# Performance work log

Hardware: AMD Instinct MI355X
Metric: run time of the kernel (lower is better)

## Reference

```python
import jax, jax.numpy as jnp
import numpy as np

N_POINTS = 2_000_000
NUM_GRAPHS = 16384
HID = 40  # ffn_param hidden_layer_size
SLOPE = 0.01  # torch default LeakyReLU negative slope


def _w(key, fan_in, fan_out):
    return jax.random.normal(key, (fan_in, fan_out), dtype=jnp.float32) / np.sqrt(fan_in)


def ffn(x, W1, W2, final_linear=False):
    # FFN with n_layers=2, bias=False, hidden=40; dropout is identity in eval.
    h = jax.nn.leaky_relu(x @ W1, SLOPE)
    h = h @ W2
    return h if final_linear else jax.nn.leaky_relu(h, SLOPE)


def setup_inputs() -> dict:
    key = jax.random.key(0)
    ks = jax.random.split(key, 10)
    x = jax.random.normal(ks[0], (N_POINTS, 3), dtype=jnp.float32)
    batch = jnp.sort(jax.random.randint(ks[1], (N_POINTS,), 0, NUM_GRAPHS)).astype(jnp.int64)
    return {
        "x": x,
        "batch": batch,
        # EPiC emb_nn: FFN(3 -> 5)
        "W_emb1": _w(ks[2], 3, HID), "W_emb2": _w(ks[3], HID, 5),
        # EPiC global_nn: FFN(5 -> 4)
        "W_glob1": _w(ks[4], 5, HID), "W_glob2": _w(ks[5], HID, 4),
        # EPiC out_nn: FFN(5+4 -> 32)
        "W_out1": _w(ks[6], 9, HID), "W_out2": _w(ks[7], HID, 32),
        # disc: FFN(32 -> 1, final_linear=True)
        "W_disc1": _w(ks[8], 32, HID), "W_disc2": _w(ks[9], HID, 1),
    }


def reference(x, batch, W_emb1, W_emb2, W_glob1, W_glob2, W_out1, W_out2, W_disc1, W_disc2):
    # EPiC block
    xe = ffn(x, W_emb1, W_emb2)                                   # [N, 5]
    x_aggr = jax.ops.segment_sum(xe, batch, num_segments=NUM_GRAPHS,
                                 indices_are_sorted=True)          # [B, 5]
    x_global = ffn(x_aggr, W_glob1, W_glob2)                       # [B, 4]
    xo = ffn(jnp.concatenate([xe, x_global[batch]], axis=-1),
             W_out1, W_out2)                                       # [N, 32]
    # global pool + final discriminator head
    pooled = jax.ops.segment_sum(xo, batch, num_segments=NUM_GRAPHS,
                                 indices_are_sorted=True)          # [B, 32]
    return ffn(pooled, W_disc1, W_disc2, final_linear=True)        # [B, 1]
```

## Files before the change

kernel.cpp:

```cpp
#include <hip/hip_runtime.h>
#include <hip/hip_bf16.h>

#define N_POINTS   2000000
#define NUM_GRAPHS 16384
#define HID        40
#define SLOPE      0.01f
#define TILE       256
#define NTILES     ((N_POINTS + TILE - 1) / TILE)
#define AROW       20
#define XOS        260

typedef __attribute__((ext_vector_type(8))) short short8;
typedef __attribute__((ext_vector_type(4))) float fx4;

__device__ __forceinline__ float lrelu(float v) { return v > 0.f ? v : SLOPE * v; }

__global__ __launch_bounds__(256) void k_emb_aggr(
    const float* __restrict__ x, const int* __restrict__ batch,
    const float* __restrict__ We1, const float* __restrict__ We2,
    float* __restrict__ x_aggr)
{
    __shared__ float sWe1[3 * HID];
    __shared__ float sWe2T[5 * HID];
    __shared__ __align__(16) float xeT[5 * XOS];
    __shared__ __align__(16) int   sb[TILE];

    int tid = threadIdx.x;
    for (int k = tid; k < 3 * HID; k += 256) sWe1[k] = We1[k];
    for (int k = tid; k < 5 * HID; k += 256) sWe2T[k] = We2[(k % HID) * 5 + k / HID];
    __syncthreads();

    for (int t = blockIdx.x; t < NTILES; t += gridDim.x) {
        int i = t * TILE + tid;
        bool v = i < N_POINTS;
        int ic = v ? i : (N_POINTS - 1);
        float x0 = x[ic * 3 + 0], x1 = x[ic * 3 + 1], x2 = x[ic * 3 + 2];
        int b = v ? batch[ic] : -1;
        sb[tid] = b;

        float h[HID];
        const float4* W1r = (const float4*)sWe1;
#pragma unroll
        for (int j4 = 0; j4 < HID / 4; ++j4) {
            float4 wa = W1r[j4], wb = W1r[10 + j4], wc = W1r[20 + j4];
            float wav[4] = {wa.x, wa.y, wa.z, wa.w};
            float wbv[4] = {wb.x, wb.y, wb.z, wb.w};
            float wcv[4] = {wc.x, wc.y, wc.z, wc.w};
#pragma unroll
            for (int k = 0; k < 4; ++k)
                h[j4 * 4 + k] = lrelu(x0 * wav[k] + x1 * wbv[k] + x2 * wcv[k]);
        }
#pragma unroll
        for (int c = 0; c < 5; ++c) {
            const float4* wr = (const float4*)&sWe2T[c * HID];
            float s = 0.f;
#pragma unroll
            for (int j4 = 0; j4 < HID / 4; ++j4) {
                float4 w = wr[j4];
                s += h[j4 * 4 + 0] * w.x + h[j4 * 4 + 1] * w.y + h[j4 * 4 + 2] * w.z + h[j4 * 4 + 3] * w.w;
            }
            xeT[c * XOS + tid] = lrelu(s);
        }
        __syncthreads();

        if (tid < 40) {
            int ch = tid >> 3, chunk = tid & 7;
            float acc = 0.f;
            int cur = sb[chunk * 32];
#pragma unroll
            for (int g = 0; g < 8; ++g) {
                float4 v4 = *(const float4*)&xeT[ch * XOS + chunk * 32 + g * 4];
                int4   n4 = *(const int4*)&sb[chunk * 32 + g * 4];
                float vv[4] = {v4.x, v4.y, v4.z, v4.w};
                int   nn[4] = {n4.x, n4.y, n4.z, n4.w};
#pragma unroll
                for (int k = 0; k < 4; ++k) {
                    if (nn[k] != cur) {
                        if (cur >= 0) atomicAdd(&x_aggr[cur * 5 + ch], acc);
                        cur = nn[k];
                        acc = vv[k];
                    } else {
                        acc += vv[k];
                    }
                }
            }
            if (cur >= 0) atomicAdd(&x_aggr[cur * 5 + ch], acc);
        }
        __syncthreads();
    }
}

__global__ __launch_bounds__(256) void k_global(
    const float* __restrict__ x_aggr,
    const float* __restrict__ Wg1, const float* __restrict__ Wg2,
    const float* __restrict__ Wo1,
    float* __restrict__ g_contrib)
{
    __shared__ float sWg1[5 * HID];
    __shared__ float sWg2[HID * 4];
    __shared__ float sWo1g[4 * HID];
    for (int k = threadIdx.x; k < 5 * HID; k += 256) sWg1[k] = Wg1[k];
    for (int k = threadIdx.x; k < HID * 4; k += 256) sWg2[k] = Wg2[k];
    for (int k = threadIdx.x; k < 4 * HID; k += 256) sWo1g[k] = Wo1[5 * HID + k];
    __syncthreads();

    int bg = blockIdx.x * 256 + threadIdx.x;
    if (bg >= NUM_GRAPHS) return;

    float a[5];
#pragma unroll
    for (int c = 0; c < 5; ++c) a[c] = x_aggr[bg * 5 + c];

    float h[HID];
#pragma unroll
    for (int j = 0; j < HID; ++j) {
        float s = 0.f;
#pragma unroll
        for (int c = 0; c < 5; ++c) s += a[c] * sWg1[c * HID + j];
        h[j] = lrelu(s);
    }
    float g[4];
#pragma unroll
    for (int c = 0; c < 4; ++c) {
        float s = 0.f;
#pragma unroll
        for (int j = 0; j < HID; ++j) s += h[j] * sWg2[j * 4 + c];
        g[c] = lrelu(s);
    }
#pragma unroll
    for (int j = 0; j < HID; ++j) {
        float s = 0.f;
#pragma unroll
        for (int c = 0; c < 4; ++c) s += g[c] * sWo1g[c * HID + j];
        g_contrib[bg * HID + j] = s;
    }
}

__global__ __launch_bounds__(256, 4) void k_out_pool(
    const float* __restrict__ x, const int* __restrict__ batch,
    const float* __restrict__ We1, const float* __restrict__ We2,
    const float* __restrict__ Wo1, const float* __restrict__ Wo2,
    const float* __restrict__ g_contrib,
    float* __restrict__ pooled)
{
    __shared__ __align__(16) unsigned int uLds[32 * XOS];
    __shared__ __align__(16) int sb[TILE];
    __shared__ float sWe1[3 * HID];
    __shared__ float sWe2T[5 * HID];
    __shared__ float sWo1[5 * HID];

    int tid = threadIdx.x;
    for (int k = tid; k < 3 * HID; k += 256) sWe1[k] = We1[k];
    for (int k = tid; k < 5 * HID; k += 256) sWe2T[k] = We2[(k % HID) * 5 + k / HID];
    for (int k = tid; k < 5 * HID; k += 256) sWo1[k] = Wo1[k];

    int lane = tid & 63;
    int l16 = lane & 15, quad = lane >> 4;

    short8 bfrag[2][2];
#pragma unroll
    for (int nt = 0; nt < 2; ++nt) {
#pragma unroll
        for (int ks = 0; ks < 2; ++ks) {
#pragma unroll
            for (int j = 0; j < 8; ++j) {
                int kk = ks * 32 + quad * 8 + j;
                float w = (kk < HID) ? Wo2[kk * 32 + nt * 16 + l16] : 0.f;
                __hip_bfloat16 hb = __float2bfloat16(w);
                bfrag[nt][ks][j] = *(short*)&hb;
            }
        }
    }
    short8 zfrag = {0, 0, 0, 0, 0, 0, 0, 0};
    __syncthreads();

    for (int t = blockIdx.x; t < NTILES; t += gridDim.x) {
        int i = t * TILE + tid;
        bool v = i < N_POINTS;
        int ic = v ? i : (N_POINTS - 1);
        float x0 = x[ic * 3 + 0], x1 = x[ic * 3 + 1], x2 = x[ic * 3 + 2];
        int b = v ? batch[ic] : -1;
        sb[tid] = b;

        float h[HID];
        const float4* W1r = (const float4*)sWe1;
#pragma unroll
        for (int j4 = 0; j4 < HID / 4; ++j4) {
            float4 wa = W1r[j4], wb = W1r[10 + j4], wc = W1r[20 + j4];
            float wav[4] = {wa.x, wa.y, wa.z, wa.w};
            float wbv[4] = {wb.x, wb.y, wb.z, wb.w};
            float wcv[4] = {wc.x, wc.y, wc.z, wc.w};
#pragma unroll
            for (int k = 0; k < 4; ++k)
                h[j4 * 4 + k] = lrelu(x0 * wav[k] + x1 * wbv[k] + x2 * wcv[k]);
        }
        float xe[5];
#pragma unroll
        for (int c = 0; c < 5; ++c) {
            const float4* wr = (const float4*)&sWe2T[c * HID];
            float s = 0.f;
#pragma unroll
            for (int j4 = 0; j4 < HID / 4; ++j4) {
                float4 w = wr[j4];
                s += h[j4 * 4 + 0] * w.x + h[j4 * 4 + 1] * w.y + h[j4 * 4 + 2] * w.z + h[j4 * 4 + 3] * w.w;
            }
            xe[c] = lrelu(s);
        }

        const float4* gc4 = (const float4*)(g_contrib + (size_t)(v ? b : 0) * HID);
        float h1v[HID];
#pragma unroll
        for (int j4 = 0; j4 < HID / 4; ++j4) {
            float4 g = gc4[j4];
            float sv[4] = {g.x, g.y, g.z, g.w};
#pragma unroll
            for (int c = 0; c < 5; ++c) {
                float4 w = ((const float4*)&sWo1[c * HID])[j4];
                float wv[4] = {w.x, w.y, w.z, w.w};
#pragma unroll
                for (int k = 0; k < 4; ++k) sv[k] += xe[c] * wv[k];
            }
#pragma unroll
            for (int k = 0; k < 4; ++k) h1v[j4 * 4 + k] = lrelu(sv[k]);
        }

        unsigned int* row = &uLds[tid * AROW];
#pragma unroll
        for (int c = 0; c < 5; ++c) {
            __hip_bfloat162 p0 = __float22bfloat162_rn(make_float2(h1v[8 * c + 0], h1v[8 * c + 1]));
            __hip_bfloat162 p1 = __float22bfloat162_rn(make_float2(h1v[8 * c + 2], h1v[8 * c + 3]));
            __hip_bfloat162 p2 = __float22bfloat162_rn(make_float2(h1v[8 * c + 4], h1v[8 * c + 5]));
            __hip_bfloat162 p3 = __float22bfloat162_rn(make_float2(h1v[8 * c + 6], h1v[8 * c + 7]));
            uint4 u;
            u.x = *(unsigned int*)&p0; u.y = *(unsigned int*)&p1;
            u.z = *(unsigned int*)&p2; u.w = *(unsigned int*)&p3;
            *(uint4*)(row + c * 4) = u;
        }

        fx4 xov[4][2];
#pragma unroll
        for (int m = 0; m < 4; ++m) {
            int mt = (tid >> 6) * 4 + m;
            const unsigned int* arow = &uLds[(mt * 16 + l16) * AROW];
            short8 a0 = *(const short8*)(arow + quad * 4);
            short8 a1 = (quad == 0) ? *(const short8*)(arow + 16) : zfrag;
#pragma unroll
            for (int nt = 0; nt < 2; ++nt) {
                fx4 acc = {0.f, 0.f, 0.f, 0.f};
                acc = __builtin_amdgcn_mfma_f32_16x16x32_bf16(a0, bfrag[nt][0], acc, 0, 0, 0);
                acc = __builtin_amdgcn_mfma_f32_16x16x32_bf16(a1, bfrag[nt][1], acc, 0, 0, 0);
#pragma unroll
                for (int r = 0; r < 4; ++r) acc[r] = lrelu(acc[r]);
                xov[m][nt] = acc;
            }
        }
        __syncthreads();

        float* xoT = (float*)uLds;
#pragma unroll
        for (int m = 0; m < 4; ++m) {
            int mt = (tid >> 6) * 4 + m;
#pragma unroll
            for (int nt = 0; nt < 2; ++nt) {
                int ch = nt * 16 + l16;
                int pt = mt * 16 + quad * 4;
                *(fx4*)&xoT[ch * XOS + pt] = xov[m][nt];
            }
        }
        __syncthreads();

        {
            int ch = tid & 31, chunk = tid >> 5;
            float acc = 0.f;
            int cur = sb[chunk * 32];
#pragma unroll
            for (int g = 0; g < 8; ++g) {
                float4 v4 = *(const float4*)&xoT[ch * XOS + chunk * 32 + g * 4];
                int4   n4 = *(const int4*)&sb[chunk * 32 + g * 4];
                float vv[4] = {v4.x, v4.y, v4.z, v4.w};
                int   nn[4] = {n4.x, n4.y, n4.z, n4.w};
#pragma unroll
                for (int k = 0; k < 4; ++k) {
                    if (nn[k] != cur) {
                        if (cur >= 0) atomicAdd(&pooled[cur * 32 + ch], acc);
                        cur = nn[k];
                        acc = vv[k];
                    } else {
                        acc += vv[k];
                    }
                }
            }
            if (cur >= 0) atomicAdd(&pooled[cur * 32 + ch], acc);
        }
        __syncthreads();
    }
}

__global__ __launch_bounds__(256) void k_disc(
    const float* __restrict__ pooled,
    const float* __restrict__ Wd1, const float* __restrict__ Wd2,
    float* __restrict__ out)
{
    __shared__ float sWd1T[HID * 32];
    __shared__ float sWd2[HID];
    for (int k = threadIdx.x; k < 32 * HID; k += 256) sWd1T[k] = Wd1[(k % 32) * HID + k / 32];
    for (int k = threadIdx.x; k < HID; k += 256) sWd2[k] = Wd2[k];
    __syncthreads();

    int bg = blockIdx.x * 256 + threadIdx.x;
    if (bg >= NUM_GRAPHS) return;

    float p[32];
    const float4* pp = (const float4*)(pooled + (size_t)bg * 32);
#pragma unroll
    for (int c4 = 0; c4 < 8; ++c4) {
        float4 vv = pp[c4];
        p[c4 * 4 + 0] = vv.x; p[c4 * 4 + 1] = vv.y; p[c4 * 4 + 2] = vv.z; p[c4 * 4 + 3] = vv.w;
    }

    float acc = 0.f;
#pragma unroll
    for (int j = 0; j < HID; ++j) {
        const float4* wr = (const float4*)&sWd1T[j * 32];
        float s = 0.f;
#pragma unroll
        for (int c4 = 0; c4 < 8; ++c4) {
            float4 w = wr[c4];
            s += p[c4 * 4 + 0] * w.x + p[c4 * 4 + 1] * w.y + p[c4 * 4 + 2] * w.z + p[c4 * 4 + 3] * w.w;
        }
        acc += lrelu(s) * sWd2[j];
    }
    out[bg] = acc;
}

extern "C" void kernel_launch(void* const* d_in, const int* in_sizes, int n_in,
                              void* d_out, int out_size, void* d_ws, size_t ws_size,
                              hipStream_t stream) {
    const float* x     = (const float*)d_in[0];
    const int*   batch = (const int*)  d_in[1];
    const float* We1   = (const float*)d_in[2];
    const float* We2   = (const float*)d_in[3];
    const float* Wg1   = (const float*)d_in[4];
    const float* Wg2   = (const float*)d_in[5];
    const float* Wo1   = (const float*)d_in[6];
    const float* Wo2   = (const float*)d_in[7];
    const float* Wd1   = (const float*)d_in[8];
    const float* Wd2   = (const float*)d_in[9];
    float* out = (float*)d_out;

    float* x_aggr    = (float*)d_ws;
    float* pooled    = x_aggr + NUM_GRAPHS * 5;
    float* g_contrib = pooled + NUM_GRAPHS * 32;

    hipMemsetAsync(d_ws, 0, (size_t)NUM_GRAPHS * (5 + 32) * sizeof(float), stream);

    int gblk = (NUM_GRAPHS + 255) / 256;
    k_emb_aggr<<<2048, 256, 0, stream>>>(x, batch, We1, We2, x_aggr);
    k_global <<<gblk, 256, 0, stream>>>(x_aggr, Wg1, Wg2, Wo1, g_contrib);
    k_out_pool<<<1024, 256, 0, stream>>>(x, batch, We1, We2, Wo1, Wo2, g_contrib, pooled);
    k_disc   <<<gblk, 256, 0, stream>>>(pooled, Wd1, Wd2, out);
}
```

Baseline: 218.7 us.

## Cache bf16 embedding outputs between kernels and process two points per thread

```diff
diff --git a/kernel.cpp b/kernel.cpp
--- a/kernel.cpp
+++ b/kernel.cpp
@@ -5,6 +5,11 @@
 #define NUM_GRAPHS 16384
 #define HID        40
 #define SLOPE      0.01f
+
+#define TILE_A     512
+#define NT_A       ((N_POINTS + TILE_A - 1) / TILE_A)
+#define XESA       584
+
 #define TILE       256
 #define NTILES     ((N_POINTS + TILE - 1) / TILE)
 #define AROW       20
@@ -14,79 +19,105 @@
 typedef __attribute__((ext_vector_type(4))) float fx4;
 
 __device__ __forceinline__ float lrelu(float v) { return v > 0.f ? v : SLOPE * v; }
-
-__global__ __launch_bounds__(256) void k_emb_aggr(
+__device__ __forceinline__ int padidx(int p) { return p + ((p >> 5) << 2); }
+__device__ __forceinline__ unsigned short f2bf(float f) {
+    __hip_bfloat16 h = __float2bfloat16(f);
+    return *(unsigned short*)&h;
+}
+__device__ __forceinline__ float bf2f(unsigned short u) {
+    unsigned int v = ((unsigned int)u) << 16;
+    return __uint_as_float(v);
+}
+
+__global__ __launch_bounds__(256, 2) void k_emb_aggr(
     const float* __restrict__ x, const int* __restrict__ batch,
     const float* __restrict__ We1, const float* __restrict__ We2,
-    float* __restrict__ x_aggr)
+    float* __restrict__ x_aggr, unsigned short* __restrict__ xe_out, int use_xe)
 {
-    __shared__ float sWe1[3 * HID];
-    __shared__ float sWe2T[5 * HID];
-    __shared__ __align__(16) float xeT[5 * XOS];
-    __shared__ __align__(16) int   sb[TILE];
+    __shared__ __align__(16) float sWe1[3 * HID];
+    __shared__ __align__(16) float sWe2T[5 * HID];
+    __shared__ __align__(16) float xeT[5 * XESA];
+    __shared__ __align__(16) int   sbp[XESA];
 
     int tid = threadIdx.x;
     for (int k = tid; k < 3 * HID; k += 256) sWe1[k] = We1[k];
     for (int k = tid; k < 5 * HID; k += 256) sWe2T[k] = We2[(k % HID) * 5 + k / HID];
     __syncthreads();
 
-    for (int t = blockIdx.x; t < NTILES; t += gridDim.x) {
-        int i = t * TILE + tid;
-        bool v = i < N_POINTS;
-        int ic = v ? i : (N_POINTS - 1);
-        float x0 = x[ic * 3 + 0], x1 = x[ic * 3 + 1], x2 = x[ic * 3 + 2];
-        int b = v ? batch[ic] : -1;
-        sb[tid] = b;
-
-        float h[HID];
-        const float4* W1r = (const float4*)sWe1;
+    int base = blockIdx.x * TILE_A;
+    int p0 = base + tid, p1 = base + 256 + tid;
+    bool v0 = p0 < N_POINTS, v1 = p1 < N_POINTS;
+    int i0 = v0 ? p0 : (N_POINTS - 1), i1 = v1 ? p1 : (N_POINTS - 1);
+    float a0 = x[i0 * 3 + 0], a1 = x[i0 * 3 + 1], a2 = x[i0 * 3 + 2];
+    float c0 = x[i1 * 3 + 0], c1 = x[i1 * 3 + 1], c2 = x[i1 * 3 + 2];
+    int b0 = v0 ? batch[i0] : -1;
+    int b1 = v1 ? batch[i1] : -1;
+    sbp[padidx(tid)] = b0;
+    sbp[padidx(256 + tid)] = b1;
+
+    float h0[HID], h1[HID];
+    const float4* W1r = (const float4*)sWe1;
+#pragma unroll
+    for (int j4 = 0; j4 < HID / 4; ++j4) {
+        float4 wa = W1r[j4], wb = W1r[10 + j4], wc = W1r[20 + j4];
+        float wav[4] = {wa.x, wa.y, wa.z, wa.w};
+        float wbv[4] = {wb.x, wb.y, wb.z, wb.w};
+        float wcv[4] = {wc.x, wc.y, wc.z, wc.w};
+#pragma unroll
+        for (int k = 0; k < 4; ++k) {
+            int j = j4 * 4 + k;
+            h0[j] = lrelu(a0 * wav[k] + a1 * wbv[k] + a2 * wcv[k]);
+            h1[j] = lrelu(c0 * wav[k] + c1 * wbv[k] + c2 * wcv[k]);
+        }
+    }
+
+#pragma unroll
+    for (int c = 0; c < 5; ++c) {
+        const float4* wr = (const float4*)&sWe2T[c * HID];
+        float s0 = 0.f, s1 = 0.f;
 #pragma unroll
         for (int j4 = 0; j4 < HID / 4; ++j4) {
-            float4 wa = W1r[j4], wb = W1r[10 + j4], wc = W1r[20 + j4];
-            float wav[4] = {wa.x, wa.y, wa.z, wa.w};
-            float wbv[4] = {wb.x, wb.y, wb.z, wb.w};
-            float wcv[4] = {wc.x, wc.y, wc.z, wc.w};
-#pragma unroll
-            for (int k = 0; k < 4; ++k)
-                h[j4 * 4 + k] = lrelu(x0 * wav[k] + x1 * wbv[k] + x2 * wcv[k]);
-        }
-#pragma unroll
-        for (int c = 0; c < 5; ++c) {
-            const float4* wr = (const float4*)&sWe2T[c * HID];
-            float s = 0.f;
-#pragma unroll
-            for (int j4 = 0; j4 < HID / 4; ++j4) {
-                float4 w = wr[j4];
-                s += h[j4 * 4 + 0] * w.x + h[j4 * 4 + 1] * w.y + h[j4 * 4 + 2] * w.z + h[j4 * 4 + 3] * w.w;
-            }
-            xeT[c * XOS + tid] = lrelu(s);
-        }
-        __syncthreads();
-
-        if (tid < 40) {
-            int ch = tid >> 3, chunk = tid & 7;
-            float acc = 0.f;
-            int cur = sb[chunk * 32];
-#pragma unroll
-            for (int g = 0; g < 8; ++g) {
-                float4 v4 = *(const float4*)&xeT[ch * XOS + chunk * 32 + g * 4];
-                int4   n4 = *(const int4*)&sb[chunk * 32 + g * 4];
-                float vv[4] = {v4.x, v4.y, v4.z, v4.w};
-                int   nn[4] = {n4.x, n4.y, n4.z, n4.w};
-#pragma unroll
-                for (int k = 0; k < 4; ++k) {
-                    if (nn[k] != cur) {
-                        if (cur >= 0) atomicAdd(&x_aggr[cur * 5 + ch], acc);
-                        cur = nn[k];
-                        acc = vv[k];
-                    } else {
-                        acc += vv[k];
-                    }
+            float4 w = wr[j4];
+            float wv[4] = {w.x, w.y, w.z, w.w};
+#pragma unroll
+            for (int k = 0; k < 4; ++k) {
+                s0 += h0[j4 * 4 + k] * wv[k];
+                s1 += h1[j4 * 4 + k] * wv[k];
+            }
+        }
+        float e0 = v0 ? lrelu(s0) : 0.f;
+        float e1 = v1 ? lrelu(s1) : 0.f;
+        xeT[c * XESA + padidx(tid)] = e0;
+        xeT[c * XESA + padidx(256 + tid)] = e1;
+        if (use_xe) {
+            if (v0) xe_out[(size_t)c * N_POINTS + p0] = f2bf(e0);
+            if (v1) xe_out[(size_t)c * N_POINTS + p1] = f2bf(e1);
+        }
+    }
+    __syncthreads();
+
+    if (tid < 80) {
+        int ch = tid >> 4, chunk = tid & 15;
+        float acc = 0.f;
+        int cur = sbp[chunk * 36];
+#pragma unroll
+        for (int g = 0; g < 8; ++g) {
+            float4 v4 = *(const float4*)&xeT[ch * XESA + chunk * 36 + g * 4];
+            int4   n4 = *(const int4*)&sbp[chunk * 36 + g * 4];
+            float vv[4] = {v4.x, v4.y, v4.z, v4.w};
+            int   nn[4] = {n4.x, n4.y, n4.z, n4.w};
+#pragma unroll
+            for (int k = 0; k < 4; ++k) {
+                if (nn[k] != cur) {
+                    if (cur >= 0) atomicAdd(&x_aggr[cur * 5 + ch], acc);
+                    cur = nn[k];
+                    acc = vv[k];
+                } else {
+                    acc += vv[k];
                 }
             }
-            if (cur >= 0) atomicAdd(&x_aggr[cur * 5 + ch], acc);
-        }
-        __syncthreads();
+        }
+        if (cur >= 0) atomicAdd(&x_aggr[cur * 5 + ch], acc);
     }
 }
 
@@ -141,6 +172,7 @@
     const float* __restrict__ We1, const float* __restrict__ We2,
     const float* __restrict__ Wo1, const float* __restrict__ Wo2,
     const float* __restrict__ g_contrib,
+    const unsigned short* __restrict__ xe_in, int use_xe,
     float* __restrict__ pooled)
 {
     __shared__ __align__(16) unsigned int uLds[32 * XOS];
@@ -166,8 +198,7 @@
             for (int j = 0; j < 8; ++j) {
                 int kk = ks * 32 + quad * 8 + j;
                 float w = (kk < HID) ? Wo2[kk * 32 + nt * 16 + l16] : 0.f;
-                __hip_bfloat16 hb = __float2bfloat16(w);
-                bfrag[nt][ks][j] = *(short*)&hb;
+                bfrag[nt][ks][j] = (short)f2bf(w);
             }
         }
     }
@@ -178,37 +209,42 @@
         int i = t * TILE + tid;
         bool v = i < N_POINTS;
         int ic = v ? i : (N_POINTS - 1);
-        float x0 = x[ic * 3 + 0], x1 = x[ic * 3 + 1], x2 = x[ic * 3 + 2];
         int b = v ? batch[ic] : -1;
         sb[tid] = b;
 
-        float h[HID];
-        const float4* W1r = (const float4*)sWe1;
-#pragma unroll
-        for (int j4 = 0; j4 < HID / 4; ++j4) {
-            float4 wa = W1r[j4], wb = W1r[10 + j4], wc = W1r[20 + j4];
-            float wav[4] = {wa.x, wa.y, wa.z, wa.w};
-            float wbv[4] = {wb.x, wb.y, wb.z, wb.w};
-            float wcv[4] = {wc.x, wc.y, wc.z, wc.w};
-#pragma unroll
-            for (int k = 0; k < 4; ++k)
-                h[j4 * 4 + k] = lrelu(x0 * wav[k] + x1 * wbv[k] + x2 * wcv[k]);
-        }
         float xe[5];
-#pragma unroll
-        for (int c = 0; c < 5; ++c) {
-            const float4* wr = (const float4*)&sWe2T[c * HID];
-            float s = 0.f;
+        if (use_xe) {
+#pragma unroll
+            for (int c = 0; c < 5; ++c) xe[c] = bf2f(xe_in[(size_t)c * N_POINTS + ic]);
+        } else {
+            float x0 = x[ic * 3 + 0], x1 = x[ic * 3 + 1], x2 = x[ic * 3 + 2];
+            float h[HID];
+            const float4* W1r = (const float4*)sWe1;
 #pragma unroll
             for (int j4 = 0; j4 < HID / 4; ++j4) {
-                float4 w = wr[j4];
-                s += h[j4 * 4 + 0] * w.x + h[j4 * 4 + 1] * w.y + h[j4 * 4 + 2] * w.z + h[j4 * 4 + 3] * w.w;
-            }
-            xe[c] = lrelu(s);
+                float4 wa = W1r[j4], wb = W1r[10 + j4], wc = W1r[20 + j4];
+                float wav[4] = {wa.x, wa.y, wa.z, wa.w};
+                float wbv[4] = {wb.x, wb.y, wb.z, wb.w};
+                float wcv[4] = {wc.x, wc.y, wc.z, wc.w};
+#pragma unroll
+                for (int k = 0; k < 4; ++k)
+                    h[j4 * 4 + k] = lrelu(x0 * wav[k] + x1 * wbv[k] + x2 * wcv[k]);
+            }
+#pragma unroll
+            for (int c = 0; c < 5; ++c) {
+                const float4* wr = (const float4*)&sWe2T[c * HID];
+                float s = 0.f;
+#pragma unroll
+                for (int j4 = 0; j4 < HID / 4; ++j4) {
+                    float4 w = wr[j4];
+                    s += h[j4 * 4 + 0] * w.x + h[j4 * 4 + 1] * w.y + h[j4 * 4 + 2] * w.z + h[j4 * 4 + 3] * w.w;
+                }
+                xe[c] = lrelu(s);
+            }
         }
 
         const float4* gc4 = (const float4*)(g_contrib + (size_t)(v ? b : 0) * HID);
-        float h1v[HID];
+        unsigned int* row = &uLds[tid * AROW];
 #pragma unroll
         for (int j4 = 0; j4 < HID / 4; ++j4) {
             float4 g = gc4[j4];
@@ -216,25 +252,15 @@
 #pragma unroll
             for (int c = 0; c < 5; ++c) {
                 float4 w = ((const float4*)&sWo1[c * HID])[j4];
-                float wv[4] = {w.x, w.y, w.z, w.w};
-#pragma unroll
-                for (int k = 0; k < 4; ++k) sv[k] += xe[c] * wv[k];
-            }
-#pragma unroll
-            for (int k = 0; k < 4; ++k) h1v[j4 * 4 + k] = lrelu(sv[k]);
-        }
-
-        unsigned int* row = &uLds[tid * AROW];
-#pragma unroll
-        for (int c = 0; c < 5; ++c) {
-            __hip_bfloat162 p0 = __float22bfloat162_rn(make_float2(h1v[8 * c + 0], h1v[8 * c + 1]));
-            __hip_bfloat162 p1 = __float22bfloat162_rn(make_float2(h1v[8 * c + 2], h1v[8 * c + 3]));
-            __hip_bfloat162 p2 = __float22bfloat162_rn(make_float2(h1v[8 * c + 4], h1v[8 * c + 5]));
-            __hip_bfloat162 p3 = __float22bfloat162_rn(make_float2(h1v[8 * c + 6], h1v[8 * c + 7]));
-            uint4 u;
-            u.x = *(unsigned int*)&p0; u.y = *(unsigned int*)&p1;
-            u.z = *(unsigned int*)&p2; u.w = *(unsigned int*)&p3;
-            *(uint4*)(row + c * 4) = u;
+                float wvv[4] = {w.x, w.y, w.z, w.w};
+#pragma unroll
+                for (int k = 0; k < 4; ++k) sv[k] += xe[c] * wvv[k];
+            }
+            __hip_bfloat162 q0 = __float22bfloat162_rn(make_float2(lrelu(sv[0]), lrelu(sv[1])));
+            __hip_bfloat162 q1 = __float22bfloat162_rn(make_float2(lrelu(sv[2]), lrelu(sv[3])));
+            uint2 u;
+            u.x = *(unsigned int*)&q0; u.y = *(unsigned int*)&q1;
+            *(uint2*)(row + j4 * 2) = u;
         }
 
         fx4 xov[4][2];
@@ -351,12 +377,17 @@
     float* x_aggr    = (float*)d_ws;
     float* pooled    = x_aggr + NUM_GRAPHS * 5;
     float* g_contrib = pooled + NUM_GRAPHS * 32;
+    size_t head_bytes = (size_t)NUM_GRAPHS * (5 + 32 + HID) * sizeof(float);
+    unsigned short* xe_ws = (unsigned short*)((char*)d_ws + head_bytes);
+    size_t need = head_bytes + (size_t)N_POINTS * 5 * sizeof(unsigned short);
+    int use_xe = (ws_size >= need) ? 1 : 0;
 
     hipMemsetAsync(d_ws, 0, (size_t)NUM_GRAPHS * (5 + 32) * sizeof(float), stream);
 
     int gblk = (NUM_GRAPHS + 255) / 256;
-    k_emb_aggr<<<2048, 256, 0, stream>>>(x, batch, We1, We2, x_aggr);
+    k_emb_aggr<<<NT_A, 256, 0, stream>>>(x, batch, We1, We2, x_aggr, xe_ws, use_xe);
     k_global <<<gblk, 256, 0, stream>>>(x_aggr, Wg1, Wg2, Wo1, g_contrib);
-    k_out_pool<<<1024, 256, 0, stream>>>(x, batch, We1, We2, Wo1, Wo2, g_contrib, pooled);
+    k_out_pool<<<1024, 256, 0, stream>>>(x, batch, We1, We2, Wo1, Wo2, g_contrib,
+                                         xe_ws, use_xe, pooled);
     k_disc   <<<gblk, 256, 0, stream>>>(pooled, Wd1, Wd2, out);
 }
```

After: 192.0 us. 12.2% less time.
